# Kernel tuning notes

Hardware: AMD Instinct MI355X
Metric: run time of the kernel (lower is better)

## Reference

```python
import jax, jax.numpy as jnp
import numpy as np

HIDDEN = 1024
HEADS = 16
HEAD_DIM = HIDDEN // HEADS
LN_EPS = 1e-6


def setup_inputs() -> dict:
    key = jax.random.key(0)
    ks = jax.random.split(key, 12)
    B, S, H = 2, 2048, HIDDEN
    s = 1.0 / np.sqrt(H)
    inp = {
        "hidden_states": jax.random.normal(ks[0], (B, S, H), dtype=jnp.float32),
        "attention_mask": jnp.ones((B, S), dtype=jnp.int32),
        "Wq": jax.random.normal(ks[1], (H, H), dtype=jnp.float32) * s,
        "bq": jax.random.normal(ks[2], (H,), dtype=jnp.float32) * 0.02,
        "Wk": jax.random.normal(ks[3], (H, H), dtype=jnp.float32) * s,
        "bk": jax.random.normal(ks[4], (H,), dtype=jnp.float32) * 0.02,
        "Wv": jax.random.normal(ks[5], (H, H), dtype=jnp.float32) * s,
        "bv": jax.random.normal(ks[6], (H,), dtype=jnp.float32) * 0.02,
        "Wo": jax.random.normal(ks[7], (H, H), dtype=jnp.float32) * s,
        "bo": jax.random.normal(ks[8], (H,), dtype=jnp.float32) * 0.02,
        "ln_g": jnp.ones((H,), dtype=jnp.float32),
        "ln_b": jnp.zeros((H,), dtype=jnp.float32),
    }
    return inp


def _split_heads(x):
    B, S, H = x.shape
    return x.reshape(B, S, HEADS, HEAD_DIM).transpose(0, 2, 1, 3)  # [B,h,S,d]


def reference(hidden_states, attention_mask, Wq, bq, Wk, bk, Wv, bv, Wo, bo, ln_g, ln_b):
    # torch nn.Linear: y = x @ W.T + b
    q = _split_heads(hidden_states @ Wq.T + bq)
    k = _split_heads(hidden_states @ Wk.T + bk)
    v = _split_heads(hidden_states @ Wv.T + bv)

    scores = jnp.einsum("bhqd,bhkd->bhqk", q, k) / np.sqrt(HEAD_DIM)
    # 2D mask path: [B,K] -> [B,1,1,K]; (1-mask)*-1e18 additive bias
    bias = (1.0 - attention_mask[:, None, None, :].astype(scores.dtype)) * -1e18
    probs = jax.nn.softmax(scores + bias, axis=-1)
    # dropout is identity in eval mode
    ctx = jnp.einsum("bhqk,bhkd->bhqd", probs, v)
    B, h, S, d = ctx.shape
    ctx = ctx.transpose(0, 2, 1, 3).reshape(B, S, h * d)

    out = ctx @ Wo.T + bo
    res = out + hidden_states
    mu = jnp.mean(res, axis=-1, keepdims=True)
    var = jnp.mean(jnp.square(res - mu), axis=-1, keepdims=True)
    return (res - mu) * jax.lax.rsqrt(var + LN_EPS) * ln_g + ln_b
```

## Files before the change

kernel.cpp:

```cpp
#include <hip/hip_runtime.h>
#include <hip/hip_bf16.h>

#define SEQ     2048
#define BATCH   2
#define HID     1024
#define NHEADS  16
#define HD      64
#define MTOT    4096
#define LNEPS   1e-6f
#define L2E     1.4426950408889634f
#define SHIFT2  26.0f

typedef __bf16 bf16_t;
typedef bf16_t bf16x8 __attribute__((ext_vector_type(8)));
typedef bf16_t bf16x4 __attribute__((ext_vector_type(4)));
typedef short  short4v __attribute__((ext_vector_type(4)));
typedef float  floatx4 __attribute__((ext_vector_type(4)));

__device__ __forceinline__ floatx4 mfma16(bf16x8 a, bf16x8 b, floatx4 c) {
    return __builtin_amdgcn_mfma_f32_16x16x32_bf16(a, b, c, 0, 0, 0);
}
__device__ __forceinline__ floatx4 mfma16k16(bf16x4 a, bf16x4 b, floatx4 c) {
    short4v as = __builtin_bit_cast(short4v, a);
    short4v bs = __builtin_bit_cast(short4v, b);
    return __builtin_amdgcn_mfma_f32_16x16x16bf16_1k(as, bs, c, 0, 0, 0);
}
__device__ __forceinline__ bf16x8 ldg8(const bf16_t* p) { return *(const bf16x8*)p; }

__device__ __forceinline__ void stage128x32(const bf16_t* __restrict__ g, int row_stride,
                                            int k0, bf16_t* lds, int wave, int lane)
{
#pragma unroll
    for (int j = 0; j < 2; j++) {
        const int rbase = wave * 32 + j * 16;
        const bf16_t* src = g + (size_t)(rbase + (lane >> 2)) * row_stride + k0 + (lane & 3) * 8;
        bf16_t* dst = lds + rbase * 32;
        __builtin_amdgcn_global_load_lds(
            (const __attribute__((address_space(1))) unsigned int*)src,
            (__attribute__((address_space(3))) unsigned int*)dst, 16, 0, 0);
    }
}
__device__ __forceinline__ void stage64x32(const bf16_t* __restrict__ g, int row_stride,
                                           int k0, bf16_t* lds, int wave, int lane)
{
    const int rbase = wave * 16;
    const bf16_t* src = g + (size_t)(rbase + (lane >> 2)) * row_stride + k0 + (lane & 3) * 8;
    bf16_t* dst = lds + rbase * 32;
    __builtin_amdgcn_global_load_lds(
        (const __attribute__((address_space(1))) unsigned int*)src,
        (__attribute__((address_space(3))) unsigned int*)dst, 16, 0, 0);
}

__global__ __launch_bounds__(256) void cvt_kernel(
    const float* sX, const float* sWq, const float* sWk, const float* sWv, const float* sWo,
    bf16_t* dX, bf16_t* dWq, bf16_t* dWk, bf16_t* dWv, bf16_t* dWo)
{
    const int z = blockIdx.z;
    const float* src; bf16_t* dst; int n;
    switch (z) {
        case 0:  src = sX;  dst = dX;  n = MTOT * HID; break;
        case 1:  src = sWq; dst = dWq; n = HID * HID;  break;
        case 2:  src = sWk; dst = dWk; n = HID * HID;  break;
        case 3:  src = sWv; dst = dWv; n = HID * HID;  break;
        default: src = sWo; dst = dWo; n = HID * HID;  break;
    }
    const int n4 = n >> 2;
    const int stride = gridDim.x * blockDim.x;
    for (int i = blockIdx.x * blockDim.x + threadIdx.x; i < n4; i += stride) {
        const float4 v = ((const float4*)src)[i];
        bf16_t o[4] = {(bf16_t)v.x, (bf16_t)v.y, (bf16_t)v.z, (bf16_t)v.w};
        *(unsigned long long*)(dst + 4 * i) = *(unsigned long long*)o;
    }
}

__global__ __launch_bounds__(256) void qkv_kernel(
    const bf16_t* __restrict__ X,
    const bf16_t* __restrict__ Wq, const float* __restrict__ bq,
    const bf16_t* __restrict__ Wk, const float* __restrict__ bk,
    const bf16_t* __restrict__ Wv, const float* __restrict__ bv,
    bf16_t* __restrict__ Qo, bf16_t* __restrict__ Ko, bf16_t* __restrict__ Vo)
{
    const int z = blockIdx.z;
    const bf16_t* W    = (z == 0) ? Wq : (z == 1) ? Wk : Wv;
    const float*  bias = (z == 0) ? bq : (z == 1) ? bk : bv;
    bf16_t*       out  = (z == 0) ? Qo : (z == 1) ? Ko : Vo;

    const int tid  = threadIdx.x;
    const int lane = tid & 63;
    const int wave = tid >> 6;
    const int l16  = lane & 15;
    const int quad = lane >> 4;
    const int m_blk = blockIdx.y * 128;
    const int n_blk = blockIdx.x * 128;
    const int m_w = (wave >> 1) * 64;
    const int n_w = (wave & 1) * 64;

    __shared__ __align__(16) char smem[18432];
    bf16_t* As = (bf16_t*)smem;
    bf16_t* Bs = (bf16_t*)(smem + 8192);

    floatx4 acc[4][4];
#pragma unroll
    for (int i = 0; i < 4; i++)
#pragma unroll
        for (int j = 0; j < 4; j++) acc[i][j] = (floatx4)0.0f;

    for (int k0 = 0; k0 < HID; k0 += 32) {
        __syncthreads();
        stage128x32(X + (size_t)m_blk * HID, HID, k0, As, wave, lane);
        stage128x32(W + (size_t)n_blk * HID, HID, k0, Bs, wave, lane);
        __syncthreads();

        bf16x8 a[4], b[4];
#pragma unroll
        for (int i = 0; i < 4; i++) a[i] = *(const bf16x8*)&As[(m_w + i * 16 + l16) * 32 + quad * 8];
#pragma unroll
        for (int j = 0; j < 4; j++) b[j] = *(const bf16x8*)&Bs[(n_w + j * 16 + l16) * 32 + quad * 8];
#pragma unroll
        for (int i = 0; i < 4; i++)
#pragma unroll
            for (int j = 0; j < 4; j++) acc[i][j] = mfma16(a[i], b[j], acc[i][j]);
    }
    __syncthreads();

    float bv_[4];
#pragma unroll
    for (int j = 0; j < 4; j++) bv_[j] = bias[n_blk + n_w + j * 16 + l16];

    bf16_t* Tw = (bf16_t*)(smem + wave * 4608);

    if (z != 2) {
        const float scale = (z == 0) ? 0.125f : 1.0f;
        const int hN = (n_blk + n_w) >> 6;
#pragma unroll
        for (int ih = 0; ih < 2; ih++) {
#pragma unroll
            for (int i2 = 0; i2 < 2; i2++) {
                const int i = ih * 2 + i2;
#pragma unroll
                for (int j = 0; j < 4; j++)
#pragma unroll
                    for (int r = 0; r < 4; r++)
                        Tw[(i2 * 16 + quad * 4 + r) * 72 + j * 16 + l16] =
                            (bf16_t)((acc[i][j][r] + bv_[j]) * scale);
            }
#pragma unroll
            for (int p = 0; p < 4; p++) {
                const int srow = p * 8 + (lane >> 3);
                const int col  = (lane & 7) * 8;
                bf16x8 v = *(const bf16x8*)&Tw[srow * 72 + col];
                const int m = m_blk + m_w + ih * 32 + srow;
                const int bb = m >> 11, s = m & (SEQ - 1);
                *(bf16x8*)&out[(((size_t)(bb * NHEADS + hN)) * SEQ + s) * HD + col] = v;
            }
        }
    } else {
        const int m0 = m_blk + m_w;
        const int bb = m0 >> 11, s0 = m0 & (SEQ - 1);
#pragma unroll
        for (int jh = 0; jh < 2; jh++) {
#pragma unroll
            for (int j2 = 0; j2 < 2; j2++) {
                const int j = jh * 2 + j2;
#pragma unroll
                for (int i = 0; i < 4; i++) {
                    bf16x4 pk;
#pragma unroll
                    for (int r = 0; r < 4; r++) pk[r] = (bf16_t)(acc[i][j][r] + bv_[j]);
                    *(bf16x4*)&Tw[(j2 * 16 + l16) * 72 + i * 16 + quad * 4] = pk;
                }
            }
#pragma unroll
            for (int p = 0; p < 4; p++) {
                const int srow = p * 8 + (lane >> 3);
                const int col  = (lane & 7) * 8;
                bf16x8 v = *(const bf16x8*)&Tw[srow * 72 + col];
                const int n = n_blk + n_w + jh * 32 + srow;
                const int h = n >> 6, d = n & 63;
                *(bf16x8*)&out[(((size_t)(bb * NHEADS + h)) * HD + d) * SEQ + s0 + col] = v;
            }
        }
    }
}

__global__ __launch_bounds__(256, 4) void attn_kernel(
    const bf16_t* __restrict__ Q, const bf16_t* __restrict__ K,
    const bf16_t* __restrict__ Vt, const int* __restrict__ mask,
    bf16_t* __restrict__ ctx)
{
    const int B   = blockIdx.x;
    const int xcd = B & 7;
    const int idx = B >> 3;
    const int bh  = xcd * 4 + (idx & 3);
    const int q0  = (idx >> 2) * 64;
    const int b   = bh >> 4;
    const int h   = bh & 15;
    const int tid  = threadIdx.x;
    const int wave = tid >> 6;
    const int lane = tid & 63;
    const int l16  = lane & 15;
    const int quad = lane >> 4;

    const bf16_t* Qh = Q  + (size_t)bh * SEQ * HD;
    const bf16_t* Kh = K  + (size_t)bh * SEQ * HD;
    const bf16_t* Vh = Vt + (size_t)bh * HD * SEQ;
    const int*    mk = mask + b * SEQ;

    __shared__ __align__(16) bf16_t Ks[64 * 72];
    __shared__ __align__(16) bf16_t Vs[64 * 72];
    __shared__ __align__(16) float  bias2[SEQ];

    for (int i = tid; i < SEQ; i += 256)
        bias2[i] = (mk[i] ? 0.0f : -1.0e30f) - SHIFT2;

    const int qw = q0 + wave * 16;

    bf16x8 bQ[2];
#pragma unroll
    for (int kc = 0; kc < 2; kc++)
        bQ[kc] = ldg8(Qh + (size_t)(qw + l16) * HD + kc * 32 + quad * 8);

    floatx4 O[4];
    floatx4 psum = (floatx4)0.0f;
#pragma unroll
    for (int dt = 0; dt < 4; dt++) O[dt] = (floatx4)0.0f;

    const int r0 = tid >> 3;
    const int c0 = (tid & 7) * 8;

    bf16x8 k0v = ldg8(Kh + (size_t)(r0)      * HD + c0);
    bf16x8 k1v = ldg8(Kh + (size_t)(32 + r0) * HD + c0);
    bf16x8 v0v = ldg8(Vh + (size_t)(r0)      * SEQ + c0);
    bf16x8 v1v = ldg8(Vh + (size_t)(32 + r0) * SEQ + c0);

    for (int kt = 0; kt < SEQ; kt += 64) {
        __syncthreads();
        *(bf16x8*)&Ks[r0 * 72 + c0]        = k0v;
        *(bf16x8*)&Ks[(32 + r0) * 72 + c0] = k1v;
        *(bf16x8*)&Vs[r0 * 72 + c0]        = v0v;
        *(bf16x8*)&Vs[(32 + r0) * 72 + c0] = v1v;
        __syncthreads();

        if (kt + 64 < SEQ) {
            k0v = ldg8(Kh + (size_t)(kt + 64 + r0)      * HD + c0);
            k1v = ldg8(Kh + (size_t)(kt + 96 + r0)      * HD + c0);
            v0v = ldg8(Vh + (size_t)(r0)      * SEQ + kt + 64 + c0);
            v1v = ldg8(Vh + (size_t)(32 + r0) * SEQ + kt + 64 + c0);
        }

#pragma unroll
        for (int kvt = 0; kvt < 4; kvt++) {
            floatx4 s = (floatx4)0.0f;
#pragma unroll
            for (int kc = 0; kc < 2; kc++) {
                bf16x8 aK = *(const bf16x8*)&Ks[(kvt * 16 + l16) * 72 + kc * 32 + quad * 8];
                s = mfma16(aK, bQ[kc], s);
            }
            const floatx4 ad = *(const floatx4*)&bias2[kt + kvt * 16 + quad * 4];
            floatx4 p;
#pragma unroll
            for (int r = 0; r < 4; r++)
                p[r] = __builtin_amdgcn_exp2f(fmaf(s[r], L2E, ad[r]));
            psum += p;
            bf16x4 pb;
#pragma unroll
            for (int r = 0; r < 4; r++) pb[r] = (bf16_t)p[r];
#pragma unroll
            for (int dt = 0; dt < 4; dt++) {
                bf16x4 aV = *(const bf16x4*)&Vs[(dt * 16 + l16) * 72 + kvt * 16 + quad * 4];
                O[dt] = mfma16k16(aV, pb, O[dt]);
            }
        }
    }

    float su = psum[0] + psum[1] + psum[2] + psum[3];
    su += __shfl_xor(su, 16, 64);
    su += __shfl_xor(su, 32, 64);
    const float linv = (su > 0.0f) ? 1.0f / su : 0.0f;

    __syncthreads();
    bf16_t* Pw = Ks + wave * 1152;
#pragma unroll
    for (int dt = 0; dt < 4; dt++) {
        floatx4 o = O[dt] * linv;
        bf16x4 pk;
#pragma unroll
        for (int r = 0; r < 4; r++) pk[r] = (bf16_t)o[r];
        *(bf16x4*)&Pw[l16 * 72 + dt * 16 + quad * 4] = pk;
    }
#pragma unroll
    for (int ch = 0; ch < 2; ch++) {
        const int cc  = ch * 64 + lane;
        const int row = cc >> 3;
        const int col = (cc & 7) * 8;
        bf16x8 vv = *(const bf16x8*)&Pw[row * 72 + col];
        *(bf16x8*)&ctx[((size_t)(b * SEQ + qw + row)) * HID + h * 64 + col] = vv;
    }
}

__global__ __launch_bounds__(256) void oproj_kernel(
    const bf16_t* __restrict__ C, const bf16_t* __restrict__ Wo,
    const float* __restrict__ bo, float* __restrict__ res)
{
    const int tid  = threadIdx.x;
    const int lane = tid & 63;
    const int wave = tid >> 6;
    const int l16  = lane & 15;
    const int quad = lane >> 4;
    const int m_blk = blockIdx.y * 64;
    const int n_blk = blockIdx.x * 128;
    const int n_w   = wave * 32;

    __shared__ __align__(16) char smem[12288];
    bf16_t* As = (bf16_t*)smem;
    bf16_t* Bs = (bf16_t*)(smem + 4096);

    floatx4 acc[4][2];
#pragma unroll
    for (int i = 0; i < 4; i++)
#pragma unroll
        for (int j = 0; j < 2; j++) acc[i][j] = (floatx4)0.0f;

    for (int k0 = 0; k0 < HID; k0 += 32) {
        __syncthreads();
        stage64x32 (C  + (size_t)m_blk * HID, HID, k0, As, wave, lane);
        stage128x32(Wo + (size_t)n_blk * HID, HID, k0, Bs, wave, lane);
        __syncthreads();

        bf16x8 a[4], b[2];
#pragma unroll
        for (int i = 0; i < 4; i++) a[i] = *(const bf16x8*)&As[(i * 16 + l16) * 32 + quad * 8];
#pragma unroll
        for (int j = 0; j < 2; j++) b[j] = *(const bf16x8*)&Bs[(n_w + j * 16 + l16) * 32 + quad * 8];
#pragma unroll
        for (int i = 0; i < 4; i++)
#pragma unroll
            for (int j = 0; j < 2; j++) acc[i][j] = mfma16(a[i], b[j], acc[i][j]);
    }
    __syncthreads();

    float bv_[2];
#pragma unroll
    for (int j = 0; j < 2; j++) bv_[j] = bo[n_blk + n_w + j * 16 + l16];

    float* Tw = (float*)(smem + wave * 2304);
#pragma unroll
    for (int ch = 0; ch < 4; ch++) {
#pragma unroll
        for (int j = 0; j < 2; j++)
#pragma unroll
            for (int r = 0; r < 4; r++)
                Tw[(quad * 4 + r) * 36 + j * 16 + l16] = acc[ch][j][r] + bv_[j];
#pragma unroll
        for (int cc = 0; cc < 2; cc++) {
            const int idx = cc * 64 + lane;
            const int row = idx >> 3;
            const int col = (idx & 7) * 4;
            float4 v = *(const float4*)&Tw[row * 36 + col];
            const int m = m_blk + ch * 16 + row;
            *(float4*)&res[(size_t)m * HID + n_blk + n_w + col] = v;
        }
    }
}

__global__ __launch_bounds__(256) void ln_kernel(
    const float* __restrict__ res, const float* __restrict__ X,
    const float* __restrict__ g, const float* __restrict__ be,
    float* __restrict__ out)
{
    __shared__ float red1[4], red2[4];
    const int row  = blockIdx.x;
    const int lane = threadIdx.x & 63;
    const int wave = threadIdx.x >> 6;
    const float4 a = ((const float4*)(res + (size_t)row * HID))[threadIdx.x];
    const float4 x = ((const float4*)(X   + (size_t)row * HID))[threadIdx.x];
    float4 v;
    v.x = a.x + x.x; v.y = a.y + x.y; v.z = a.z + x.z; v.w = a.w + x.w;

    float s = v.x + v.y + v.z + v.w;
#pragma unroll
    for (int off = 1; off < 64; off <<= 1) s += __shfl_xor(s, off, 64);
    if (lane == 0) red1[wave] = s;
    __syncthreads();
    const float mu = (red1[0] + red1[1] + red1[2] + red1[3]) * (1.0f / HID);

    const float d0 = v.x - mu, d1 = v.y - mu, d2 = v.z - mu, d3 = v.w - mu;
    float ss = d0 * d0 + d1 * d1 + d2 * d2 + d3 * d3;
#pragma unroll
    for (int off = 1; off < 64; off <<= 1) ss += __shfl_xor(ss, off, 64);
    if (lane == 0) red2[wave] = ss;
    __syncthreads();
    const float var = (red2[0] + red2[1] + red2[2] + red2[3]) * (1.0f / HID);
    const float rstd = rsqrtf(var + LNEPS);

    const float4 gv = ((const float4*)g)[threadIdx.x];
    const float4 bv = ((const float4*)be)[threadIdx.x];
    float4 o;
    o.x = d0 * rstd * gv.x + bv.x;
    o.y = d1 * rstd * gv.y + bv.y;
    o.z = d2 * rstd * gv.z + bv.z;
    o.w = d3 * rstd * gv.w + bv.w;
    ((float4*)(out + (size_t)row * HID))[threadIdx.x] = o;
}

extern "C" void kernel_launch(void* const* d_in, const int* in_sizes, int n_in,
                              void* d_out, int out_size, void* d_ws, size_t ws_size,
                              hipStream_t stream)
{
    const float* X  = (const float*)d_in[0];
    const int* mask = (const int*)d_in[1];
    const float* Wq = (const float*)d_in[2];  const float* bq = (const float*)d_in[3];
    const float* Wk = (const float*)d_in[4];  const float* bk = (const float*)d_in[5];
    const float* Wv = (const float*)d_in[6];  const float* bv = (const float*)d_in[7];
    const float* Wo = (const float*)d_in[8];  const float* bo = (const float*)d_in[9];
    const float* g  = (const float*)d_in[10]; const float* be = (const float*)d_in[11];
    float* out = (float*)d_out;

    char* ws = (char*)d_ws;
    bf16_t* Qb  = (bf16_t*)(ws);
    bf16_t* Kb  = (bf16_t*)(ws + (8ull  << 20));
    bf16_t* Vb  = (bf16_t*)(ws + (16ull << 20));
    bf16_t* Cb  = (bf16_t*)(ws + (24ull << 20));
    float*  Rb  = (float*)(ws);
    bf16_t* Xc  = (bf16_t*)(ws + (32ull << 20));
    bf16_t* Wqc = (bf16_t*)(ws + (40ull << 20));
    bf16_t* Wkc = (bf16_t*)(ws + (42ull << 20));
    bf16_t* Wvc = (bf16_t*)(ws + (44ull << 20));
    bf16_t* Woc = (bf16_t*)(ws + (46ull << 20));

    cvt_kernel <<<dim3(128, 1, 5), 256, 0, stream>>>(X, Wq, Wk, Wv, Wo, Xc, Wqc, Wkc, Wvc, Woc);
    qkv_kernel <<<dim3(8, 32, 3), 256, 0, stream>>>(Xc, Wqc, bq, Wkc, bk, Wvc, bv, Qb, Kb, Vb);
    attn_kernel<<<dim3(32 * 32), 256, 0, stream>>>(Qb, Kb, Vb, mask, Cb);
    oproj_kernel<<<dim3(8, 64), 256, 0, stream>>>(Cb, Woc, bo, Rb);
    ln_kernel  <<<MTOT, 256, 0, stream>>>(Rb, X, g, be, out);
}
```

Baseline: 143.7 us.

## Process two query tiles per wave and XOR-swizzle K/V shared memory

Each attention wave now handles 32 query rows instead of 16, so every K and V fragment read from shared memory feeds two MFMA streams, and the grid is halved to 512 blocks of 128 queries. K and V tiles drop the padded 72-element stride for XOR-swizzled 128-byte rows to avoid LDS bank conflicts, with V written as split 4-element halves. This raises register pressure (doubled accumulators, launch-bounds occupancy hint removed) and gives fewer blocks to spread across CUs.

```diff
diff --git a/kernel.cpp b/kernel.cpp
--- a/kernel.cpp
+++ b/kernel.cpp
@@ -183,7 +183,7 @@
     }
 }
 
-__global__ __launch_bounds__(256, 4) void attn_kernel(
+__global__ __launch_bounds__(256) void attn_kernel(
     const bf16_t* __restrict__ Q, const bf16_t* __restrict__ K,
     const bf16_t* __restrict__ Vt, const int* __restrict__ mask,
     bf16_t* __restrict__ ctx)
@@ -192,7 +192,7 @@
     const int xcd = B & 7;
     const int idx = B >> 3;
     const int bh  = xcd * 4 + (idx & 3);
-    const int q0  = (idx >> 2) * 64;
+    const int q0  = (idx >> 2) * 128;
     const int b   = bh >> 4;
     const int h   = bh & 15;
     const int tid  = threadIdx.x;
@@ -200,33 +200,49 @@
     const int lane = tid & 63;
     const int l16  = lane & 15;
     const int quad = lane >> 4;
+    const int r7   = l16 & 7;
 
     const bf16_t* Qh = Q  + (size_t)bh * SEQ * HD;
     const bf16_t* Kh = K  + (size_t)bh * SEQ * HD;
     const bf16_t* Vh = Vt + (size_t)bh * HD * SEQ;
     const int*    mk = mask + b * SEQ;
 
-    __shared__ __align__(16) bf16_t Ks[64 * 72];
-    __shared__ __align__(16) bf16_t Vs[64 * 72];
-    __shared__ __align__(16) float  bias2[SEQ];
+    __shared__ __align__(16) char smem[24576];
+    bf16_t* Ks    = (bf16_t*)smem;
+    bf16_t* Vs    = (bf16_t*)(smem + 8192);
+    float*  bias2 = (float*)(smem + 16384);
 
     for (int i = tid; i < SEQ; i += 256)
         bias2[i] = (mk[i] ? 0.0f : -1.0e30f) - SHIFT2;
 
-    const int qw = q0 + wave * 16;
-
-    bf16x8 bQ[2];
-#pragma unroll
-    for (int kc = 0; kc < 2; kc++)
-        bQ[kc] = ldg8(Qh + (size_t)(qw + l16) * HD + kc * 32 + quad * 8);
-
-    floatx4 O[4];
-    floatx4 psum = (floatx4)0.0f;
-#pragma unroll
-    for (int dt = 0; dt < 4; dt++) O[dt] = (floatx4)0.0f;
+    const int qw = q0 + wave * 32;
+
+    bf16x8 bQ[2][2];
+#pragma unroll
+    for (int qh = 0; qh < 2; qh++)
+#pragma unroll
+        for (int kc = 0; kc < 2; kc++)
+            bQ[qh][kc] = ldg8(Qh + (size_t)(qw + qh * 16 + l16) * HD + kc * 32 + quad * 8);
+
+    floatx4 O[2][4];
+    floatx4 psum[2];
+#pragma unroll
+    for (int qh = 0; qh < 2; qh++) {
+        psum[qh] = (floatx4)0.0f;
+#pragma unroll
+        for (int dt = 0; dt < 4; dt++) O[qh][dt] = (floatx4)0.0f;
+    }
 
     const int r0 = tid >> 3;
-    const int c0 = (tid & 7) * 8;
+    const int cK = tid & 7;
+    const int c0 = cK * 8;
+    const int wofsK = r0 * 128 + ((cK ^ (r0 & 7)) << 4);
+    const int vr  = r0 & 15;
+    const int vg0 = (((cK << 1)    ) ^ vr) << 3;
+    const int vg1 = (((cK << 1) + 1) ^ vr) << 3;
+    const int kb0 = l16 * 128 + (((quad    ) ^ r7) << 4);
+    const int kb1 = l16 * 128 + (((4 + quad) ^ r7) << 4);
+    const int vbase = l16 * 128;
 
     bf16x8 k0v = ldg8(Kh + (size_t)(r0)      * HD + c0);
     bf16x8 k1v = ldg8(Kh + (size_t)(32 + r0) * HD + c0);
@@ -235,66 +251,83 @@
 
     for (int kt = 0; kt < SEQ; kt += 64) {
         __syncthreads();
-        *(bf16x8*)&Ks[r0 * 72 + c0]        = k0v;
-        *(bf16x8*)&Ks[(32 + r0) * 72 + c0] = k1v;
-        *(bf16x8*)&Vs[r0 * 72 + c0]        = v0v;
-        *(bf16x8*)&Vs[(32 + r0) * 72 + c0] = v1v;
+        *(bf16x8*)((char*)Ks + wofsK)        = k0v;
+        *(bf16x8*)((char*)Ks + wofsK + 4096) = k1v;
+        {
+            char* vrow = (char*)Vs + r0 * 128;
+            bf16x4 lo0 = __builtin_shufflevector(v0v, v0v, 0, 1, 2, 3);
+            bf16x4 hi0 = __builtin_shufflevector(v0v, v0v, 4, 5, 6, 7);
+            bf16x4 lo1 = __builtin_shufflevector(v1v, v1v, 0, 1, 2, 3);
+            bf16x4 hi1 = __builtin_shufflevector(v1v, v1v, 4, 5, 6, 7);
+            *(bf16x4*)(vrow + vg0)        = lo0;
+            *(bf16x4*)(vrow + vg1)        = hi0;
+            *(bf16x4*)(vrow + 4096 + vg0) = lo1;
+            *(bf16x4*)(vrow + 4096 + vg1) = hi1;
+        }
         __syncthreads();
 
         if (kt + 64 < SEQ) {
-            k0v = ldg8(Kh + (size_t)(kt + 64 + r0)      * HD + c0);
-            k1v = ldg8(Kh + (size_t)(kt + 96 + r0)      * HD + c0);
+            k0v = ldg8(Kh + (size_t)(kt + 64 + r0) * HD + c0);
+            k1v = ldg8(Kh + (size_t)(kt + 96 + r0) * HD + c0);
             v0v = ldg8(Vh + (size_t)(r0)      * SEQ + kt + 64 + c0);
             v1v = ldg8(Vh + (size_t)(32 + r0) * SEQ + kt + 64 + c0);
         }
 
 #pragma unroll
         for (int kvt = 0; kvt < 4; kvt++) {
-            floatx4 s = (floatx4)0.0f;
-#pragma unroll
-            for (int kc = 0; kc < 2; kc++) {
-                bf16x8 aK = *(const bf16x8*)&Ks[(kvt * 16 + l16) * 72 + kc * 32 + quad * 8];
-                s = mfma16(aK, bQ[kc], s);
-            }
+            bf16x8 aK0 = *(const bf16x8*)((char*)Ks + kb0 + kvt * 2048);
+            bf16x8 aK1 = *(const bf16x8*)((char*)Ks + kb1 + kvt * 2048);
             const floatx4 ad = *(const floatx4*)&bias2[kt + kvt * 16 + quad * 4];
-            floatx4 p;
-#pragma unroll
-            for (int r = 0; r < 4; r++)
-                p[r] = __builtin_amdgcn_exp2f(fmaf(s[r], L2E, ad[r]));
-            psum += p;
-            bf16x4 pb;
-#pragma unroll
-            for (int r = 0; r < 4; r++) pb[r] = (bf16_t)p[r];
+            bf16x4 pb[2];
+#pragma unroll
+            for (int qh = 0; qh < 2; qh++) {
+                floatx4 s = (floatx4)0.0f;
+                s = mfma16(aK0, bQ[qh][0], s);
+                s = mfma16(aK1, bQ[qh][1], s);
+                floatx4 p;
+#pragma unroll
+                for (int r = 0; r < 4; r++)
+                    p[r] = __builtin_amdgcn_exp2f(fmaf(s[r], L2E, ad[r]));
+                psum[qh] += p;
+#pragma unroll
+                for (int r = 0; r < 4; r++) pb[qh][r] = (bf16_t)p[r];
+            }
+            const int vofs = vbase + ((((kvt << 2) + quad) ^ l16) << 3);
 #pragma unroll
             for (int dt = 0; dt < 4; dt++) {
-                bf16x4 aV = *(const bf16x4*)&Vs[(dt * 16 + l16) * 72 + kvt * 16 + quad * 4];
-                O[dt] = mfma16k16(aV, pb, O[dt]);
-            }
-        }
-    }
-
-    float su = psum[0] + psum[1] + psum[2] + psum[3];
-    su += __shfl_xor(su, 16, 64);
-    su += __shfl_xor(su, 32, 64);
-    const float linv = (su > 0.0f) ? 1.0f / su : 0.0f;
+                bf16x4 aV = *(const bf16x4*)((char*)Vs + vofs + dt * 2048);
+                O[0][dt] = mfma16k16(aV, pb[0], O[0][dt]);
+                O[1][dt] = mfma16k16(aV, pb[1], O[1][dt]);
+            }
+        }
+    }
 
     __syncthreads();
-    bf16_t* Pw = Ks + wave * 1152;
-#pragma unroll
-    for (int dt = 0; dt < 4; dt++) {
-        floatx4 o = O[dt] * linv;
-        bf16x4 pk;
-#pragma unroll
-        for (int r = 0; r < 4; r++) pk[r] = (bf16_t)o[r];
-        *(bf16x4*)&Pw[l16 * 72 + dt * 16 + quad * 4] = pk;
-    }
-#pragma unroll
-    for (int ch = 0; ch < 2; ch++) {
-        const int cc  = ch * 64 + lane;
-        const int row = cc >> 3;
-        const int col = (cc & 7) * 8;
-        bf16x8 vv = *(const bf16x8*)&Pw[row * 72 + col];
-        *(bf16x8*)&ctx[((size_t)(b * SEQ + qw + row)) * HID + h * 64 + col] = vv;
+
+#pragma unroll
+    for (int qh = 0; qh < 2; qh++) {
+        float su = psum[qh][0] + psum[qh][1] + psum[qh][2] + psum[qh][3];
+        su += __shfl_xor(su, 16, 64);
+        su += __shfl_xor(su, 32, 64);
+        const float linv = (su > 0.0f) ? 1.0f / su : 0.0f;
+
+        bf16_t* Pw = (bf16_t*)(smem + wave * 4608 + qh * 2304);
+#pragma unroll
+        for (int dt = 0; dt < 4; dt++) {
+            floatx4 o = O[qh][dt] * linv;
+            bf16x4 pk;
+#pragma unroll
+            for (int r = 0; r < 4; r++) pk[r] = (bf16_t)o[r];
+            *(bf16x4*)&Pw[l16 * 72 + dt * 16 + quad * 4] = pk;
+        }
+#pragma unroll
+        for (int ch = 0; ch < 2; ch++) {
+            const int cc  = ch * 64 + lane;
+            const int row = cc >> 3;
+            const int col = (cc & 7) * 8;
+            bf16x8 vv = *(const bf16x8*)&Pw[row * 72 + col];
+            *(bf16x8*)&ctx[((size_t)(b * SEQ + qw + qh * 16 + row)) * HID + h * 64 + col] = vv;
+        }
     }
 }
 
@@ -430,7 +463,7 @@
 
     cvt_kernel <<<dim3(128, 1, 5), 256, 0, stream>>>(X, Wq, Wk, Wv, Wo, Xc, Wqc, Wkc, Wvc, Woc);
     qkv_kernel <<<dim3(8, 32, 3), 256, 0, stream>>>(Xc, Wqc, bq, Wkc, bk, Wvc, bv, Qb, Kb, Vb);
-    attn_kernel<<<dim3(32 * 32), 256, 0, stream>>>(Qb, Kb, Vb, mask, Cb);
+    attn_kernel<<<dim3(512), 256, 0, stream>>>(Qb, Kb, Vb, mask, Cb);
     oproj_kernel<<<dim3(8, 64), 256, 0, stream>>>(Cb, Woc, bo, Rb);
     ln_kernel  <<<MTOT, 256, 0, stream>>>(Rb, X, g, be, out);
 }
```

Measured after the change: 134.7 us. 6.3% less time.
